# Performance work log

Measured on AMD Instinct MI355X. Metric: run time of the kernel, lower is better.

Reference implementation:

```python
import jax, jax.numpy as jnp
import numpy as np

# Gate hyperparameters (match init_kwargs)
DIM = 2048
TOPK = 2
N_EXPERT = 8
ROUTE_SCALE = 1.0
ALPHA = 0.1  # score_func = 'softmax', training = True


def setup_inputs() -> dict:
    key = jax.random.key(0)
    kx, kw = jax.random.split(key)
    B, N = 4, 4096
    x = jax.random.normal(kx, (B, N, DIM), dtype=jnp.float32)
    # nn.Linear(dim, n_route_expert, bias=False) -> weight shape (E, D)
    W = jax.random.normal(kw, (N_EXPERT, DIM), dtype=jnp.float32) * 0.02
    return {"x": x, "W": W}


def reference(x, W):
    b, n, d = x.shape
    xf = x.reshape(-1, d)                      # (b*n, D)
    score = jax.nn.softmax(xf @ W.T, axis=-1)  # (b*n, E)
    weight, idx = jax.lax.top_k(score, TOPK)   # (b*n, K) each

    # aux load-balancing loss (training branch)
    # fi: per-batch expert hit frequency via scatter_add of ones
    onehot = jax.nn.one_hot(idx.reshape(b, n * TOPK), N_EXPERT, dtype=score.dtype)
    fi = onehot.sum(axis=1) * (N_EXPERT / (TOPK * n))   # (b, E)
    pi = score.reshape(b, n, N_EXPERT).mean(axis=1)     # (b, E)
    aux_loss = (fi * pi).sum(axis=1).mean() * ALPHA

    weight = weight * ROUTE_SCALE
    return weight, idx, aux_loss
```

## Files before the change

### kernel.cpp

```cpp
#include <hip/hip_runtime.h>
#include <hip/hip_bf16.h>

#define TOKENS    16384
#define DIM       2048
#define NEXP      8
#define NBATCH    4
#define TOK_PER_B 4096
#define ALPHA     0.1f
#define NBLK      256
#define TPB       64
#define CHUNK     128
#define NCHUNK    16

typedef const __attribute__((address_space(1))) unsigned int* gas_t;
typedef __attribute__((address_space(3))) unsigned int* las_t;


__global__ __launch_bounds__(1024, 1)
void gate_kernel(const float* __restrict__ x, const float* __restrict__ W,
                 float* __restrict__ out, float* __restrict__ ws)
{
    __shared__ float Wl[NEXP * DIM];
    __shared__ float xs[2][16][4 * CHUNK];
    __shared__ float s_part[16][NEXP];
    __shared__ float s_pcnt[16][NEXP];

    const int tid  = threadIdx.x;
    const int lane = tid & 63;
    const int wavu = __builtin_amdgcn_readfirstlane(tid >> 6);
    const int tok0 = blockIdx.x * TPB + wavu * 4;

    #pragma unroll
    for (int i = 0; i < 4; ++i) {
        const float* src = W + wavu * 1024 + i * 256 + lane * 4;
        __builtin_amdgcn_global_load_lds((gas_t)src,
                                         (las_t)(Wl + wavu * 1024 + i * 256), 16, 0, 0);
    }
    {
        const float* srow = x + (size_t)tok0 * DIM + 0 * CHUNK;
        #pragma unroll
        for (int d = 0; d < 2; ++d)
            __builtin_amdgcn_global_load_lds(
                (gas_t)(srow + (size_t)(2 * d + (lane >> 5)) * DIM + (lane & 31) * 4),
                (las_t)(&xs[0][wavu][0] + d * 256), 16, 0, 0);
    }
    asm volatile("s_waitcnt vmcnt(2)" ::: "memory");
    __builtin_amdgcn_sched_barrier(0);
    __syncthreads();

    float acc[4][NEXP];
    #pragma unroll
    for (int t = 0; t < 4; ++t)
        #pragma unroll
        for (int e = 0; e < NEXP; ++e) acc[t][e] = 0.f;

    #pragma unroll 1
    for (int c = 0; c < NCHUNK; ++c) {
        const int cb = c & 1;
        if (c < NCHUNK - 1) {
            const float* srow = x + (size_t)tok0 * DIM + (c + 1) * CHUNK;
            #pragma unroll
            for (int d = 0; d < 2; ++d)
                __builtin_amdgcn_global_load_lds(
                    (gas_t)(srow + (size_t)(2 * d + (lane >> 5)) * DIM + (lane & 31) * 4),
                    (las_t)(&xs[cb ^ 1][wavu][0] + d * 256), 16, 0, 0);
            asm volatile("s_waitcnt vmcnt(2)" ::: "memory");
        } else {
            asm volatile("s_waitcnt vmcnt(0)" ::: "memory");
        }
        __builtin_amdgcn_sched_barrier(0);

        const float* xsl = &xs[cb][wavu][0];
        float2 xv[4];
        #pragma unroll
        for (int t = 0; t < 4; ++t)
            xv[t] = *(const float2*)&xsl[t * CHUNK + lane * 2];
        #pragma unroll
        for (int e = 0; e < NEXP; e += 2) {
            float2 w0 = *(const float2*)&Wl[(e    ) * DIM + c * CHUNK + lane * 2];
            float2 w1 = *(const float2*)&Wl[(e + 1) * DIM + c * CHUNK + lane * 2];
            #pragma unroll
            for (int t = 0; t < 4; ++t) {
                acc[t][e]     += xv[t].x * w0.x + xv[t].y * w0.y;
                acc[t][e + 1] += xv[t].x * w1.x + xv[t].y * w1.y;
            }
        }
    }

    const bool b0 = lane & 1;
    const bool b1 = lane & 2;
    const bool b2 = lane & 4;
    const bool b4 = lane & 16;
    const bool b5 = lane & 32;
    const int  myexp = lane & 7;
    const int  grp8  = (lane >> 3) * 8;
    const int  myj   = ((lane >> 4) & 1) * 2 + ((lane >> 5) & 1);

    float r[4];
    #pragma unroll
    for (int j = 0; j < 4; ++j) {
        float m0 = b0 ? acc[j][1] : acc[j][0], s0 = b0 ? acc[j][0] : acc[j][1];
        float m1 = b0 ? acc[j][3] : acc[j][2], s1 = b0 ? acc[j][2] : acc[j][3];
        float m2 = b0 ? acc[j][5] : acc[j][4], s2 = b0 ? acc[j][4] : acc[j][5];
        float m3 = b0 ? acc[j][7] : acc[j][6], s3 = b0 ? acc[j][6] : acc[j][7];
        float k0 = m0 + __shfl_xor(s0, 1, 64);
        float k1 = m1 + __shfl_xor(s1, 1, 64);
        float k2 = m2 + __shfl_xor(s2, 1, 64);
        float k3 = m3 + __shfl_xor(s3, 1, 64);
        float n0 = b1 ? k1 : k0, q0 = b1 ? k0 : k1;
        float n1 = b1 ? k3 : k2, q1 = b1 ? k2 : k3;
        float h0 = n0 + __shfl_xor(q0, 2, 64);
        float h1 = n1 + __shfl_xor(q1, 2, 64);
        float nm = b2 ? h1 : h0, nq = b2 ? h0 : h1;
        float rj = nm + __shfl_xor(nq, 4, 64);
        r[j] = rj + __shfl_xor(rj, 8, 64);
    }
    float a_  = b4 ? r[2] : r[0], as_ = b4 ? r[0] : r[2];
    float bb  = b4 ? r[3] : r[1], bs_ = b4 ? r[1] : r[3];
    a_ += __shfl_xor(as_, 16, 64);
    bb += __shfl_xor(bs_, 16, 64);
    float sel = b5 ? bb : a_, snd = b5 ? a_ : bb;
    float rr  = sel + __shfl_xor(snd, 32, 64);

    float m = rr;
    m = fmaxf(m, __shfl_xor(m, 1, 64));
    m = fmaxf(m, __shfl_xor(m, 2, 64));
    m = fmaxf(m, __shfl_xor(m, 4, 64));
    float p = __expf(rr - m);
    float s = p;
    s += __shfl_xor(s, 1, 64);
    s += __shfl_xor(s, 2, 64);
    s += __shfl_xor(s, 4, 64);
    float inv = 1.0f / s;

    unsigned long long bm = __ballot(rr == m);
    int i0 = __ffs((unsigned)((bm >> grp8) & 0xffULL)) - 1;
    float rm = (myexp == i0) ? -3.4e38f : rr;
    float mm = rm;
    mm = fmaxf(mm, __shfl_xor(mm, 1, 64));
    mm = fmaxf(mm, __shfl_xor(mm, 2, 64));
    mm = fmaxf(mm, __shfl_xor(mm, 4, 64));
    unsigned long long bm2 = __ballot(rm == mm);
    int i1 = __ffs((unsigned)((bm2 >> grp8) & 0xffULL)) - 1;

    float v0 = inv;
    float v1 = __expf(mm - m) * inv;

    float pacc = (lane & 8) ? 0.f : p * inv;
    float cacc = (lane & 8) ? 0.f : ((myexp == i0 ? 1.f : 0.f) + (myexp == i1 ? 1.f : 0.f));
    pacc += __shfl_xor(pacc, 8, 64);
    pacc += __shfl_xor(pacc, 16, 64);
    pacc += __shfl_xor(pacc, 32, 64);
    cacc += __shfl_xor(cacc, 8, 64);
    cacc += __shfl_xor(cacc, 16, 64);
    cacc += __shfl_xor(cacc, 32, 64);

    if ((lane & 15) == 0) {
        const int t = tok0 + myj;
        out[(size_t)t * 2 + 0] = v0;
        out[(size_t)t * 2 + 1] = v1;
        out[(size_t)TOKENS * 2 + (size_t)t * 2 + 0] = (float)i0;
        out[(size_t)TOKENS * 2 + (size_t)t * 2 + 1] = (float)i1;
    }

    if (lane < NEXP) {
        s_part[wavu][lane] = pacc;
        s_pcnt[wavu][lane] = cacc;
    }
    __syncthreads();
    if (tid < NEXP) {
        float sp = 0.f, sc = 0.f;
        #pragma unroll
        for (int w = 0; w < 16; ++w) { sp += s_part[w][tid]; sc += s_pcnt[w][tid]; }
        ws[blockIdx.x * 16 + tid]     = sp;
        ws[blockIdx.x * 16 + 8 + tid] = sc;
    }
}

__global__ void finalize_kernel(const float* __restrict__ ws, float* __restrict__ out)
{
    __shared__ float red[256];
    __shared__ float fin[64];
    const int tid  = threadIdx.x;
    const int cell = tid >> 2;
    const int q    = tid & 3;
    const int b    = cell >> 4;
    const int c    = cell & 15;

    float acc = 0.f;
    #pragma unroll
    for (int k = 0; k < 16; ++k)
        acc += ws[(size_t)(b * 64 + q + k * 4) * 16 + c];
    red[cell * 4 + q] = acc;
    __syncthreads();

    if (tid < 64)
        fin[tid] = red[tid * 4] + red[tid * 4 + 1] + red[tid * 4 + 2] + red[tid * 4 + 3];
    __syncthreads();

    if (tid == 0) {
        float aux = 0.f;
        for (int bb = 0; bb < NBATCH; ++bb) {
            float a2 = 0.f;
            for (int e = 0; e < NEXP; ++e) {
                float pi = fin[bb * 16 + e] * (1.f / TOK_PER_B);
                float fi = fin[bb * 16 + 8 + e] * ((float)NEXP / (2.f * TOK_PER_B));
                a2 += fi * pi;
            }
            aux += a2;
        }
        out[(size_t)TOKENS * 4] = aux * (1.f / NBATCH) * ALPHA;
    }
}

extern "C" void kernel_launch(void* const* d_in, const int* in_sizes, int n_in,
                              void* d_out, int out_size, void* d_ws, size_t ws_size,
                              hipStream_t stream) {
    const float* x = (const float*)d_in[0];
    const float* W = (const float*)d_in[1];
    float* out = (float*)d_out;
    float* ws  = (float*)d_ws;

    gate_kernel<<<dim3(NBLK), dim3(1024), 0, stream>>>(x, W, out, ws);
    finalize_kernel<<<1, 256, 0, stream>>>(ws, out);
}
```

Baseline: 31.45 us.

## Load x directly into registers and fuse finalize into gate via last-block atomic

Replaces the async global-to-LDS double-buffered x staging with register prefetch of float4 rows, and widens each chunk to 256 floats. The W copy to LDS becomes a plain vectorized load. The separate finalize kernel is folded into the gate kernel: the last block, found with an atomic counter, performs the aux-loss reduction. This removes a kernel launch but adds a memset launch and a threadfence/atomic tail.

```diff
diff --git a/kernel.cpp b/kernel.cpp
--- a/kernel.cpp
+++ b/kernel.cpp
@@ -9,44 +9,42 @@
 #define ALPHA     0.1f
 #define NBLK      256
 #define TPB       64
-#define CHUNK     128
-#define NCHUNK    16
-
-typedef const __attribute__((address_space(1))) unsigned int* gas_t;
-typedef __attribute__((address_space(3))) unsigned int* las_t;
-
+#define CHUNK     256
+#define NCHUNK    8
+
+
+__device__ __forceinline__ float dot4(float4 a, float4 b) {
+    return a.x * b.x + a.y * b.y + a.z * b.z + a.w * b.w;
+}
 
 __global__ __launch_bounds__(1024, 1)
 void gate_kernel(const float* __restrict__ x, const float* __restrict__ W,
-                 float* __restrict__ out, float* __restrict__ ws)
+                 float* __restrict__ out, float* __restrict__ ws,
+                 unsigned int* __restrict__ cnt)
 {
     __shared__ float Wl[NEXP * DIM];
-    __shared__ float xs[2][16][4 * CHUNK];
     __shared__ float s_part[16][NEXP];
     __shared__ float s_pcnt[16][NEXP];
+    __shared__ float red[256];
+    __shared__ float fin[64];
+    __shared__ unsigned int s_last;
 
     const int tid  = threadIdx.x;
     const int lane = tid & 63;
     const int wavu = __builtin_amdgcn_readfirstlane(tid >> 6);
     const int tok0 = blockIdx.x * TPB + wavu * 4;
 
-    #pragma unroll
-    for (int i = 0; i < 4; ++i) {
-        const float* src = W + wavu * 1024 + i * 256 + lane * 4;
-        __builtin_amdgcn_global_load_lds((gas_t)src,
-                                         (las_t)(Wl + wavu * 1024 + i * 256), 16, 0, 0);
-    }
     {
-        const float* srow = x + (size_t)tok0 * DIM + 0 * CHUNK;
-        #pragma unroll
-        for (int d = 0; d < 2; ++d)
-            __builtin_amdgcn_global_load_lds(
-                (gas_t)(srow + (size_t)(2 * d + (lane >> 5)) * DIM + (lane & 31) * 4),
-                (las_t)(&xs[0][wavu][0] + d * 256), 16, 0, 0);
-    }
-    asm volatile("s_waitcnt vmcnt(2)" ::: "memory");
-    __builtin_amdgcn_sched_barrier(0);
+        const float4* W4 = (const float4*)W;
+        float4*       Wd = (float4*)Wl;
+        #pragma unroll
+        for (int i = 0; i < 4; ++i)
+            Wd[tid + i * 1024] = W4[tid + i * 1024];
+    }
     __syncthreads();
+
+    const float4* xr  = (const float4*)(x + (size_t)tok0 * DIM);
+    const float4* Wl4 = (const float4*)Wl;
 
     float acc[4][NEXP];
     #pragma unroll
@@ -54,36 +52,30 @@
         #pragma unroll
         for (int e = 0; e < NEXP; ++e) acc[t][e] = 0.f;
 
+    float4 xc[4], xn[4];
+    #pragma unroll
+    for (int t = 0; t < 4; ++t) xc[t] = xr[t * (DIM / 4) + lane];
+
     #pragma unroll 1
     for (int c = 0; c < NCHUNK; ++c) {
-        const int cb = c & 1;
         if (c < NCHUNK - 1) {
-            const float* srow = x + (size_t)tok0 * DIM + (c + 1) * CHUNK;
-            #pragma unroll
-            for (int d = 0; d < 2; ++d)
-                __builtin_amdgcn_global_load_lds(
-                    (gas_t)(srow + (size_t)(2 * d + (lane >> 5)) * DIM + (lane & 31) * 4),
-                    (las_t)(&xs[cb ^ 1][wavu][0] + d * 256), 16, 0, 0);
-            asm volatile("s_waitcnt vmcnt(2)" ::: "memory");
-        } else {
-            asm volatile("s_waitcnt vmcnt(0)" ::: "memory");
-        }
-        __builtin_amdgcn_sched_barrier(0);
-
-        const float* xsl = &xs[cb][wavu][0];
-        float2 xv[4];
-        #pragma unroll
-        for (int t = 0; t < 4; ++t)
-            xv[t] = *(const float2*)&xsl[t * CHUNK + lane * 2];
+            #pragma unroll
+            for (int t = 0; t < 4; ++t)
+                xn[t] = xr[t * (DIM / 4) + (c + 1) * 64 + lane];
+        }
         #pragma unroll
         for (int e = 0; e < NEXP; e += 2) {
-            float2 w0 = *(const float2*)&Wl[(e    ) * DIM + c * CHUNK + lane * 2];
-            float2 w1 = *(const float2*)&Wl[(e + 1) * DIM + c * CHUNK + lane * 2];
+            float4 w0 = Wl4[(e    ) * (DIM / 4) + c * 64 + lane];
+            float4 w1 = Wl4[(e + 1) * (DIM / 4) + c * 64 + lane];
             #pragma unroll
             for (int t = 0; t < 4; ++t) {
-                acc[t][e]     += xv[t].x * w0.x + xv[t].y * w0.y;
-                acc[t][e + 1] += xv[t].x * w1.x + xv[t].y * w1.y;
+                acc[t][e]     += dot4(xc[t], w0);
+                acc[t][e + 1] += dot4(xc[t], w1);
             }
+        }
+        if (c < NCHUNK - 1) {
+            #pragma unroll
+            for (int t = 0; t < 4; ++t) xc[t] = xn[t];
         }
     }
 
@@ -175,41 +167,43 @@
         ws[blockIdx.x * 16 + tid]     = sp;
         ws[blockIdx.x * 16 + 8 + tid] = sc;
     }
-}
-
-__global__ void finalize_kernel(const float* __restrict__ ws, float* __restrict__ out)
-{
-    __shared__ float red[256];
-    __shared__ float fin[64];
-    const int tid  = threadIdx.x;
-    const int cell = tid >> 2;
-    const int q    = tid & 3;
-    const int b    = cell >> 4;
-    const int c    = cell & 15;
-
-    float acc = 0.f;
-    #pragma unroll
-    for (int k = 0; k < 16; ++k)
-        acc += ws[(size_t)(b * 64 + q + k * 4) * 16 + c];
-    red[cell * 4 + q] = acc;
+
+    __threadfence();
+    if (tid == 0) {
+        unsigned int old = atomicAdd(cnt, 1u);
+        s_last = (old == NBLK - 1) ? 1u : 0u;
+    }
     __syncthreads();
-
-    if (tid < 64)
-        fin[tid] = red[tid * 4] + red[tid * 4 + 1] + red[tid * 4 + 2] + red[tid * 4 + 3];
-    __syncthreads();
-
-    if (tid == 0) {
-        float aux = 0.f;
-        for (int bb = 0; bb < NBATCH; ++bb) {
+    if (s_last) {
+        __threadfence();
+        const int cell = tid >> 2;
+        const int q    = tid & 3;
+        const int b    = cell >> 4;
+        const int c    = cell & 15;
+        if (tid < 256) {
             float a2 = 0.f;
-            for (int e = 0; e < NEXP; ++e) {
-                float pi = fin[bb * 16 + e] * (1.f / TOK_PER_B);
-                float fi = fin[bb * 16 + 8 + e] * ((float)NEXP / (2.f * TOK_PER_B));
-                a2 += fi * pi;
+            #pragma unroll
+            for (int k = 0; k < 16; ++k)
+                a2 += ws[(size_t)(b * 64 + q + k * 4) * 16 + c];
+            red[cell * 4 + q] = a2;
+        }
+        __syncthreads();
+        if (tid < 64)
+            fin[tid] = red[tid * 4] + red[tid * 4 + 1] + red[tid * 4 + 2] + red[tid * 4 + 3];
+        __syncthreads();
+        if (tid == 0) {
+            float aux = 0.f;
+            for (int bb2 = 0; bb2 < NBATCH; ++bb2) {
+                float a2 = 0.f;
+                for (int e = 0; e < NEXP; ++e) {
+                    float pi = fin[bb2 * 16 + e] * (1.f / TOK_PER_B);
+                    float fi = fin[bb2 * 16 + 8 + e] * ((float)NEXP / (2.f * TOK_PER_B));
+                    a2 += fi * pi;
+                }
+                aux += a2;
             }
-            aux += a2;
-        }
-        out[(size_t)TOKENS * 4] = aux * (1.f / NBATCH) * ALPHA;
+            out[(size_t)TOKENS * 4] = aux * (1.f / NBATCH) * ALPHA;
+        }
     }
 }
 
@@ -220,7 +214,9 @@
     const float* W = (const float*)d_in[1];
     float* out = (float*)d_out;
     float* ws  = (float*)d_ws;
-
-    gate_kernel<<<dim3(NBLK), dim3(1024), 0, stream>>>(x, W, out, ws);
-    finalize_kernel<<<1, 256, 0, stream>>>(ws, out);
+    unsigned int* cnt = (unsigned int*)(ws + NBLK * 16);
+
+    hipMemsetAsync((void*)cnt, 0, sizeof(unsigned int), stream);
+
+    gate_kernel<<<dim3(NBLK), dim3(1024), 0, stream>>>(x, W, out, ws, cnt);
 }
```

Result: slower. 96.04 us (+205.3%).
